# Kernel optimization log

Measured on AMD Instinct MI355X. Metric: run time of the kernel, lower is better.

## Reference

```python
import jax, jax.numpy as jnp
import numpy as np

STEP = 0.01  # matches init kwarg step=0.01


def _disc(x, step=STEP):
    """Discretize like pd.cut with bins arange(floor(min), ceil(max)+step, step).
    Bin identity is all that matters for entropy, so we return integer bin ids.
    (Boundary convention: half-open floor binning; pd.cut uses right-closed,
    which differs only on exact bin edges - measure-zero for continuous data.)"""
    lower = jnp.floor(jnp.min(x))
    return jnp.floor((x - lower) / step).astype(jnp.int32)


def _row_joint_entropy(labels_list):
    """Per-row empirical (joint) entropy in nats of discrete label tuples.
    H_row = -sum_v p_v log p_v = -(1/n) * sum_i log(count(x_i)/n),
    computed via pairwise-equality counts (vectorized Counter).
    labels_list: list of [B, n] int arrays. Returns [B]."""
    eq = None
    for lab in labels_list:
        e = lab[:, :, None] == lab[:, None, :]  # [B, n, n]
        eq = e if eq is None else (eq & e)
    n = labels_list[0].shape[1]
    counts = eq.sum(-1).astype(jnp.float32)  # [B, n]
    return -jnp.mean(jnp.log(counts / n), axis=-1)  # [B]


def _h_soft(o, d):
    """F.cross_entropy(o, softmax(d), 'mean') - F.kl_div(log_softmax(o), softmax(d), 'mean').
    Note torch kl_div 'mean' averages over ALL elements (B*C)."""
    p = jax.nn.softmax(d, axis=-1)
    logq = jax.nn.log_softmax(o, axis=-1)
    ce = -jnp.mean(jnp.sum(p * logq, axis=-1))          # mean over batch
    kl = jnp.mean(p * (jnp.log(p) - logq))               # mean over B*C
    return ce - kl


def reference(data, data1, data2, data3, output1, output2, output3, output):
    # --- reconstruction term ---
    mse_loss = 0.5 * jnp.mean((data - output) ** 2)

    # --- discrete entropies on detached inputs (torch: .detach().numpy()) ---
    d1 = _disc(jax.lax.stop_gradient(data1))
    d2 = _disc(jax.lax.stop_gradient(data2))
    d3 = _disc(jax.lax.stop_gradient(data3))

    H_data_1 = jnp.mean(_row_joint_entropy([d1]))
    H_data_2 = jnp.mean(_row_joint_entropy([d2]))
    H_data_3 = jnp.mean(_row_joint_entropy([d3]))

    H_output_1 = _h_soft(output1, data1)
    H_output_2 = _h_soft(output2, data2)
    H_output_3 = _h_soft(output3, data3)

    H_1 = H_data_1 - H_output_1
    H_2 = H_data_2 - H_output_2
    H_3 = H_data_3 - H_output_3

    # equal widths -> pad_matrices is a no-op
    H_in_1_3 = jnp.mean(_row_joint_entropy([d1, d3]))
    H_in_2_3 = jnp.mean(_row_joint_entropy([d2, d3]))
    H_in_1_2 = jnp.mean(_row_joint_entropy([d1, d2]))

    in1_3 = jnp.concatenate((data1, data3), axis=1)
    in2_3 = jnp.concatenate((data2, data3), axis=1)
    in1_2 = jnp.concatenate((data1, data2), axis=1)
    out1_3 = jnp.concatenate((output1, output3), axis=1)
    out2_3 = jnp.concatenate((output2, output3), axis=1)
    out1_2 = jnp.concatenate((output1, output2), axis=1)

    H_out_1_3 = _h_soft(out1_3, in1_3)
    H_out_2_3 = _h_soft(out2_3, in2_3)
    H_out_1_2 = _h_soft(out1_2, in1_2)

    data1_3 = H_data_1 + H_data_3 - H_in_1_3
    data2_3 = H_data_2 + H_data_3 - H_in_2_3
    data1_2 = H_data_1 + H_data_2 - H_in_1_2
    label1_3 = H_output_1 + H_output_3 - H_out_1_3
    label2_3 = H_output_2 + H_output_3 - H_out_2_3
    label1_2 = H_output_1 + H_output_2 - H_out_1_2

    H_MI1_3 = label1_3 - data1_3
    H_MI2_3 = label2_3 - data2_3
    H_MI1_2 = label1_2 - data1_2

    # per-row conditional MI I(X1; X2 | X3) = H(X1,X3)+H(X2,X3)-H(X3)-H(X1,X2,X3),
    # summed over rows (torch loop accumulates cmi per row without averaging)
    cmi_rows = (_row_joint_entropy([d1, d3]) + _row_joint_entropy([d2, d3])
                - _row_joint_entropy([d3]) - _row_joint_entropy([d1, d2, d3]))
    ave_data_ConMI = jnp.sum(cmi_rows)

    in123 = jnp.concatenate((data1, data2, data3), axis=1)
    out123 = jnp.concatenate((output1, output2, output3), axis=1)
    H_output_123 = _h_soft(out123, in123)
    ave_label_ConMI = H_out_2_3 - H_output_3 + H_out_1_3 - H_output_123
    CMI = ave_label_ConMI - ave_data_ConMI

    return (0.5 * mse_loss
            + 0.25 * (jnp.square(H_1) + jnp.square(H_2) + jnp.square(H_3))
            + 0.25 * (jnp.square(H_MI1_3) + jnp.square(H_MI2_3)
                      + jnp.square(H_MI1_2) + jnp.square(CMI)))


def setup_inputs() -> dict:
    key = jax.random.key(0)
    ks = jax.random.split(key, 8)
    B, D, DT = 2048, 256, 768
    return {
        "data": jax.random.normal(ks[0], (B, DT), dtype=jnp.float32),
        "data1": jax.random.normal(ks[1], (B, D), dtype=jnp.float32),
        "data2": jax.random.normal(ks[2], (B, D), dtype=jnp.float32),
        "data3": jax.random.normal(ks[3], (B, D), dtype=jnp.float32),
        "output1": jax.random.normal(ks[4], (B, D), dtype=jnp.float32),
        "output2": jax.random.normal(ks[5], (B, D), dtype=jnp.float32),
        "output3": jax.random.normal(ks[6], (B, D), dtype=jnp.float32),
        "output": jax.random.normal(ks[7], (B, DT), dtype=jnp.float32),
    }
```

## Files before the change

kernel.cpp:

```cpp
#include <hip/hip_runtime.h>
#include <math.h>

#define B_ROWS 2048
#define NCOL   256
#define DTOT   768
#define BANKS  16
#define HSLOTS 512


#define LO (-6.0f)

__global__ __launch_bounds__(256)
void zero_kernel(double* __restrict__ acc) {
    for (int z = threadIdx.x; z < BANKS * 22; z += 256) acc[z] = 0.0;
}

__device__ __forceinline__ int hslot0(unsigned key) {
    return (int)((key * 0x9E3779B1u) >> 23);
}

__device__ __forceinline__ int hfix(unsigned* __restrict__ h, int slot,
                                    unsigned key, unsigned prev) {
    while (true) {
        if (prev == 0u) return slot;
        if ((prev >> 10) == key) { atomicAdd(&h[slot], 1u); return slot; }
        slot = (slot + 1) & (HSLOTS - 1);
        prev = atomicCAS(&h[slot], 0u, (key << 10) + 1u);
    }
}

__global__ __launch_bounds__(64)
void row_kernel(const float* __restrict__ d1, const float* __restrict__ d2,
                const float* __restrict__ d3,
                const float* __restrict__ o1, const float* __restrict__ o2,
                const float* __restrict__ o3,
                const float* __restrict__ data, const float* __restrict__ outp,
                double* __restrict__ acc) {
    __shared__ unsigned ht[7][HSLOTS];

    const int r = blockIdx.x, lane = threadIdx.x;

    {
        uint4* h4 = (uint4*)&ht[0][0];
        #pragma unroll
        for (int z = 0; z < 14; ++z) h4[lane + z * 64] = make_uint4(0u, 0u, 0u, 0u);
    }

    const float4 X1 = ((const float4*)(d1 + r * NCOL))[lane];
    const float4 X2 = ((const float4*)(d2 + r * NCOL))[lane];
    const float4 X3 = ((const float4*)(d3 + r * NCOL))[lane];
    const float4 Y1 = ((const float4*)(o1 + r * NCOL))[lane];
    const float4 Y2 = ((const float4*)(o2 + r * NCOL))[lane];
    const float4 Y3 = ((const float4*)(o3 + r * NCOL))[lane];
    const float x1[4] = {X1.x, X1.y, X1.z, X1.w};
    const float x2[4] = {X2.x, X2.y, X2.z, X2.w};
    const float x3[4] = {X3.x, X3.y, X3.z, X3.w};
    const float y1[4] = {Y1.x, Y1.y, Y1.z, Y1.w};
    const float y2[4] = {Y2.x, Y2.y, Y2.z, Y2.w};
    const float y3[4] = {Y3.x, Y3.y, Y3.z, Y3.w};

    float ms = 0.f;
    #pragma unroll
    for (int t = 0; t < 3; ++t) {
        const float4 a = ((const float4*)(data + r * DTOT))[lane + 64 * t];
        const float4 o = ((const float4*)(outp + r * DTOT))[lane + 64 * t];
        const float dx = a.x - o.x, dy = a.y - o.y, dz = a.z - o.z, dw = a.w - o.w;
        ms += dx * dx + dy * dy + dz * dz + dw * dw;
    }
    __syncthreads();

    unsigned* t0 = ht[0]; unsigned* t1 = ht[1]; unsigned* t2 = ht[2];
    unsigned* t3 = ht[3]; unsigned* t4 = ht[4]; unsigned* t5 = ht[5];
    unsigned* t6 = ht[6];

    int SL[4][7];
    float sv[12] = {0,0,0,0,0,0,0,0,0,0,0,0};
    #pragma unroll
    for (int j = 0; j < 4; ++j) {
        const unsigned k1 = (unsigned)(int)floorf((x1[j] - LO) / 0.01f);
        const unsigned k2 = (unsigned)(int)floorf((x2[j] - LO) / 0.01f);
        const unsigned k3 = (unsigned)(int)floorf((x3[j] - LO) / 0.01f);
        const unsigned k13 = k1 | (k3 << 11), k23 = k2 | (k3 << 11), k12 = k1 | (k2 << 11);
        int s1 = hslot0(k1), s2 = hslot0(k2), s3 = hslot0(k3);
        int s13 = hslot0(k13), s23 = hslot0(k23), s12 = hslot0(k12);
        const unsigned p1  = atomicCAS(&t0[s1],  0u, (k1  << 10) + 1u);
        const unsigned p2  = atomicCAS(&t1[s2],  0u, (k2  << 10) + 1u);
        const unsigned p3  = atomicCAS(&t2[s3],  0u, (k3  << 10) + 1u);
        const unsigned p13 = atomicCAS(&t3[s13], 0u, (k13 << 10) + 1u);
        const unsigned p23 = atomicCAS(&t4[s23], 0u, (k23 << 10) + 1u);
        const unsigned p12 = atomicCAS(&t5[s12], 0u, (k12 << 10) + 1u);
        SL[j][0] = hfix(t0, s1,  k1,  p1);
        SL[j][1] = hfix(t1, s2,  k2,  p2);
        SL[j][2] = hfix(t2, s3,  k3,  p3);
        s13 = hfix(t3, s13, k13, p13);
        SL[j][3] = s13;
        SL[j][4] = hfix(t4, s23, k23, p23);
        SL[j][5] = hfix(t5, s12, k12, p12);
        const unsigned k123 = (unsigned)s13 | (k2 << 9);
        int s123 = hslot0(k123);
        const unsigned p123 = atomicCAS(&t6[s123], 0u, (k123 << 10) + 1u);
        SL[j][6] = hfix(t6, s123, k123, p123);

        const float ed1 = __expf(x1[j]), ed2 = __expf(x2[j]), ed3 = __expf(x3[j]);
        sv[0] += ed1; sv[1] += ed1 * y1[j]; sv[2]  += ed1 * x1[j]; sv[3]  += __expf(y1[j]);
        sv[4] += ed2; sv[5] += ed2 * y2[j]; sv[6]  += ed2 * x2[j]; sv[7]  += __expf(y2[j]);
        sv[8] += ed3; sv[9] += ed3 * y3[j]; sv[10] += ed3 * x3[j]; sv[11] += __expf(y3[j]);
    }

    float logacc[7] = {0,0,0,0,0,0,0};
    #pragma unroll
    for (int j = 0; j < 4; ++j) {
        logacc[0] += __logf((float)(t0[SL[j][0]] & 1023u));
        logacc[1] += __logf((float)(t1[SL[j][1]] & 1023u));
        logacc[2] += __logf((float)(t2[SL[j][2]] & 1023u));
        logacc[3] += __logf((float)(t3[SL[j][3]] & 1023u));
        logacc[4] += __logf((float)(t4[SL[j][4]] & 1023u));
        logacc[5] += __logf((float)(t5[SL[j][5]] & 1023u));
        logacc[6] += __logf((float)(t6[SL[j][6]] & 1023u));
    }

    float svt[12];
    #pragma unroll
    for (int s = 0; s < 12; ++s) {
        float x = sv[s];
        for (int off = 32; off; off >>= 1) x += __shfl_xor(x, off);
        svt[s] = x;
    }
    float lgt[7];
    #pragma unroll
    for (int s = 0; s < 7; ++s) {
        float x = logacc[s];
        for (int off = 32; off; off >>= 1) x += __shfl_xor(x, off);
        lgt[s] = x;
    }
    float mst = ms;
    for (int off = 32; off; off >>= 1) mst += __shfl_xor(mst, off);

    float fin = mst;
    if (lane < 7) {
        #pragma unroll
        for (int s = 0; s < 7; ++s) fin = (lane == s) ? lgt[s] : fin;
    } else if (lane < 21) {
        const int mi = (lane < 14) ? lane - 7 : lane - 14;
        const int M[7] = {1, 2, 4, 5, 6, 3, 7};
        int mk = 0;
        #pragma unroll
        for (int s = 0; s < 7; ++s) mk = (mi == s) ? M[s] : mk;
        float Zd = 0.f, Td = 0.f, Ud = 0.f, Zo = 0.f;
        #pragma unroll
        for (int k = 0; k < 3; ++k) {
            const float c = (float)((mk >> k) & 1);
            Zd += c * svt[4*k]; Td += c * svt[4*k+1];
            Ud += c * svt[4*k+2]; Zo += c * svt[4*k+3];
        }
        const float Ld = __logf(Zd), Lo = __logf(Zo);
        const float Spo = Td / Zd, Spd = Ud / Zd;
        fin = (lane < 14) ? (Lo - Spo) : ((Spd - Ld) - (Spo - Lo));
    }
    if (lane < 22) atomicAdd(&acc[(r & (BANKS - 1)) * 22 + lane], (double)fin);
}

__global__ __launch_bounds__(64)
void fold_kernel(const double* __restrict__ acc, float* __restrict__ out) {
    __shared__ double T[22];
    const int lane = threadIdx.x;
    if (lane < 22) {
        double s = 0.0;
        #pragma unroll
        for (int bk = 0; bk < BANKS; ++bk) s += acc[bk * 22 + lane];
        T[lane] = s;
    }
    __syncthreads();
    if (lane == 0) {
        const double n = 256.0, Bd = 2048.0;
        const double logn = log(n);
        const double S1 = T[0], S2 = T[1], S3 = T[2];
        const double S13 = T[3], S23 = T[4], S12 = T[5], S123 = T[6];
        const double Hd1   = logn - S1  / (Bd * n);
        const double Hd2   = logn - S2  / (Bd * n);
        const double Hd3   = logn - S3  / (Bd * n);
        const double Hin13 = logn - S13 / (Bd * n);
        const double Hin23 = logn - S23 / (Bd * n);
        const double Hin12 = logn - S12 / (Bd * n);
        const double C[7] = {256, 256, 256, 512, 512, 512, 768};
        double Ho[7];
        for (int m = 0; m < 7; ++m) Ho[m] = T[7 + m] / Bd - T[14 + m] / (Bd * C[m]);
        const double H1 = Hd1 - Ho[0], H2 = Hd2 - Ho[1], H3 = Hd3 - Ho[2];
        const double MI13 = (Ho[0] + Ho[2] - Ho[3]) - (Hd1 + Hd3 - Hin13);
        const double MI23 = (Ho[1] + Ho[2] - Ho[4]) - (Hd2 + Hd3 - Hin23);
        const double MI12 = (Ho[0] + Ho[1] - Ho[5]) - (Hd1 + Hd2 - Hin12);
        const double aveD = -(S13 + S23 - S3 - S123) / n;
        const double aveL = Ho[4] - Ho[2] + Ho[3] - Ho[6];
        const double CMI = aveL - aveD;
        const double mse = 0.5 * T[21] / (Bd * 768.0);
        out[0] = (float)(0.5 * mse
                       + 0.25 * (H1 * H1 + H2 * H2 + H3 * H3)
                       + 0.25 * (MI13 * MI13 + MI23 * MI23 + MI12 * MI12
                                 + CMI * CMI));
    }
}

extern "C" void kernel_launch(void* const* d_in, const int* in_sizes, int n_in,
                              void* d_out, int out_size, void* d_ws, size_t ws_size,
                              hipStream_t stream) {
    const float* data = (const float*)d_in[0];
    const float* d1   = (const float*)d_in[1];
    const float* d2   = (const float*)d_in[2];
    const float* d3   = (const float*)d_in[3];
    const float* o1   = (const float*)d_in[4];
    const float* o2   = (const float*)d_in[5];
    const float* o3   = (const float*)d_in[6];
    const float* outp = (const float*)d_in[7];

    double* acc = (double*)d_ws;

    zero_kernel<<<1, 256, 0, stream>>>(acc);
    row_kernel<<<B_ROWS, 64, 0, stream>>>(d1, d2, d3, o1, o2, o3, data, outp, acc);
    fold_kernel<<<1, 64, 0, stream>>>(acc, (float*)d_out);
}
```

Measured before the change: 102.9 us.

## Use 256-thread blocks per row and write per-row partials instead of atomics

Each row is now processed by 256 threads, one element per thread, instead of 64 threads handling four elements each. The per-row results are reduced through shared memory and written to a per-row workspace slot rather than atomically added into banked double accumulators. This removes the zero kernel and the global double atomics, and the fold kernel now reduces 2048 values per statistic with a 512-thread block. In exchange it adds extra block-wide syncs, uses scalar rather than vector loads, and puts more hash-table contention on each row's 256 threads.

```diff
diff --git a/kernel.cpp b/kernel.cpp
--- a/kernel.cpp
+++ b/kernel.cpp
@@ -4,16 +4,10 @@
 #define B_ROWS 2048
 #define NCOL   256
 #define DTOT   768
-#define BANKS  16
 #define HSLOTS 512
 
-
 #define LO (-6.0f)
 
-__global__ __launch_bounds__(256)
-void zero_kernel(double* __restrict__ acc) {
-    for (int z = threadIdx.x; z < BANKS * 22; z += 256) acc[z] = 0.0;
-}
 
 __device__ __forceinline__ int hslot0(unsigned key) {
     return (int)((key * 0x9E3779B1u) >> 23);
@@ -29,43 +23,39 @@
     }
 }
 
-__global__ __launch_bounds__(64)
+__global__ __launch_bounds__(256)
 void row_kernel(const float* __restrict__ d1, const float* __restrict__ d2,
                 const float* __restrict__ d3,
                 const float* __restrict__ o1, const float* __restrict__ o2,
                 const float* __restrict__ o3,
                 const float* __restrict__ data, const float* __restrict__ outp,
-                double* __restrict__ acc) {
+                double* __restrict__ ws) {
     __shared__ unsigned ht[7][HSLOTS];
-
-    const int r = blockIdx.x, lane = threadIdx.x;
-
-    {
-        uint4* h4 = (uint4*)&ht[0][0];
-        #pragma unroll
-        for (int z = 0; z < 14; ++z) h4[lane + z * 64] = make_uint4(0u, 0u, 0u, 0u);
-    }
-
-    const float4 X1 = ((const float4*)(d1 + r * NCOL))[lane];
-    const float4 X2 = ((const float4*)(d2 + r * NCOL))[lane];
-    const float4 X3 = ((const float4*)(d3 + r * NCOL))[lane];
-    const float4 Y1 = ((const float4*)(o1 + r * NCOL))[lane];
-    const float4 Y2 = ((const float4*)(o2 + r * NCOL))[lane];
-    const float4 Y3 = ((const float4*)(o3 + r * NCOL))[lane];
-    const float x1[4] = {X1.x, X1.y, X1.z, X1.w};
-    const float x2[4] = {X2.x, X2.y, X2.z, X2.w};
-    const float x3[4] = {X3.x, X3.y, X3.z, X3.w};
-    const float y1[4] = {Y1.x, Y1.y, Y1.z, Y1.w};
-    const float y2[4] = {Y2.x, Y2.y, Y2.z, Y2.w};
-    const float y3[4] = {Y3.x, Y3.y, Y3.z, Y3.w};
+    __shared__ float tot[20];
+
+    const int r = blockIdx.x, tid = threadIdx.x;
+    const int lane = tid & 63;
+
+    const float x1 = d1[r * NCOL + tid];
+    const float x2 = d2[r * NCOL + tid];
+    const float x3 = d3[r * NCOL + tid];
+    const float y1 = o1[r * NCOL + tid];
+    const float y2 = o2[r * NCOL + tid];
+    const float y3 = o3[r * NCOL + tid];
 
     float ms = 0.f;
     #pragma unroll
     for (int t = 0; t < 3; ++t) {
-        const float4 a = ((const float4*)(data + r * DTOT))[lane + 64 * t];
-        const float4 o = ((const float4*)(outp + r * DTOT))[lane + 64 * t];
-        const float dx = a.x - o.x, dy = a.y - o.y, dz = a.z - o.z, dw = a.w - o.w;
-        ms += dx * dx + dy * dy + dz * dz + dw * dw;
+        const float a = data[r * DTOT + tid + 256 * t];
+        const float o = outp[r * DTOT + tid + 256 * t];
+        const float dd = a - o;
+        ms += dd * dd;
+    }
+
+    {
+        uint4* h4 = (uint4*)&ht[0][0];
+        for (int z = tid; z < 7 * HSLOTS / 4; z += 256)
+            h4[z] = make_uint4(0u, 0u, 0u, 0u);
     }
     __syncthreads();
 
@@ -73,105 +63,110 @@
     unsigned* t3 = ht[3]; unsigned* t4 = ht[4]; unsigned* t5 = ht[5];
     unsigned* t6 = ht[6];
 
-    int SL[4][7];
-    float sv[12] = {0,0,0,0,0,0,0,0,0,0,0,0};
+    const unsigned k1 = (unsigned)(int)floorf((x1 - LO) / 0.01f);
+    const unsigned k2 = (unsigned)(int)floorf((x2 - LO) / 0.01f);
+    const unsigned k3 = (unsigned)(int)floorf((x3 - LO) / 0.01f);
+    const unsigned k13 = k1 | (k3 << 11), k23 = k2 | (k3 << 11), k12 = k1 | (k2 << 11);
+    int s1 = hslot0(k1), s2 = hslot0(k2), s3 = hslot0(k3);
+    int s13 = hslot0(k13), s23 = hslot0(k23), s12 = hslot0(k12);
+    const unsigned p1  = atomicCAS(&t0[s1],  0u, (k1  << 10) + 1u);
+    const unsigned p2  = atomicCAS(&t1[s2],  0u, (k2  << 10) + 1u);
+    const unsigned p3  = atomicCAS(&t2[s3],  0u, (k3  << 10) + 1u);
+    const unsigned p13 = atomicCAS(&t3[s13], 0u, (k13 << 10) + 1u);
+    const unsigned p23 = atomicCAS(&t4[s23], 0u, (k23 << 10) + 1u);
+    const unsigned p12 = atomicCAS(&t5[s12], 0u, (k12 << 10) + 1u);
+    const int SL0 = hfix(t0, s1,  k1,  p1);
+    const int SL1 = hfix(t1, s2,  k2,  p2);
+    const int SL2 = hfix(t2, s3,  k3,  p3);
+    const int SL3 = hfix(t3, s13, k13, p13);
+    const int SL4 = hfix(t4, s23, k23, p23);
+    const int SL5 = hfix(t5, s12, k12, p12);
+    const unsigned k123 = (unsigned)SL3 | (k2 << 9);
+    int s123 = hslot0(k123);
+    const unsigned p123 = atomicCAS(&t6[s123], 0u, (k123 << 10) + 1u);
+    const int SL6 = hfix(t6, s123, k123, p123);
+
+    float vals[20];
+    const float e1 = __expf(x1), e2 = __expf(x2), e3 = __expf(x3);
+    vals[7]  = e1; vals[8]  = e1 * y1; vals[9]  = e1 * x1; vals[10] = __expf(y1);
+    vals[11] = e2; vals[12] = e2 * y2; vals[13] = e2 * x2; vals[14] = __expf(y2);
+    vals[15] = e3; vals[16] = e3 * y3; vals[17] = e3 * x3; vals[18] = __expf(y3);
+    vals[19] = ms;
+
+    __syncthreads();
+
+    vals[0] = __logf((float)(t0[SL0] & 1023u));
+    vals[1] = __logf((float)(t1[SL1] & 1023u));
+    vals[2] = __logf((float)(t2[SL2] & 1023u));
+    vals[3] = __logf((float)(t3[SL3] & 1023u));
+    vals[4] = __logf((float)(t4[SL4] & 1023u));
+    vals[5] = __logf((float)(t5[SL5] & 1023u));
+    vals[6] = __logf((float)(t6[SL6] & 1023u));
+
     #pragma unroll
-    for (int j = 0; j < 4; ++j) {
-        const unsigned k1 = (unsigned)(int)floorf((x1[j] - LO) / 0.01f);
-        const unsigned k2 = (unsigned)(int)floorf((x2[j] - LO) / 0.01f);
-        const unsigned k3 = (unsigned)(int)floorf((x3[j] - LO) / 0.01f);
-        const unsigned k13 = k1 | (k3 << 11), k23 = k2 | (k3 << 11), k12 = k1 | (k2 << 11);
-        int s1 = hslot0(k1), s2 = hslot0(k2), s3 = hslot0(k3);
-        int s13 = hslot0(k13), s23 = hslot0(k23), s12 = hslot0(k12);
-        const unsigned p1  = atomicCAS(&t0[s1],  0u, (k1  << 10) + 1u);
-        const unsigned p2  = atomicCAS(&t1[s2],  0u, (k2  << 10) + 1u);
-        const unsigned p3  = atomicCAS(&t2[s3],  0u, (k3  << 10) + 1u);
-        const unsigned p13 = atomicCAS(&t3[s13], 0u, (k13 << 10) + 1u);
-        const unsigned p23 = atomicCAS(&t4[s23], 0u, (k23 << 10) + 1u);
-        const unsigned p12 = atomicCAS(&t5[s12], 0u, (k12 << 10) + 1u);
-        SL[j][0] = hfix(t0, s1,  k1,  p1);
-        SL[j][1] = hfix(t1, s2,  k2,  p2);
-        SL[j][2] = hfix(t2, s3,  k3,  p3);
-        s13 = hfix(t3, s13, k13, p13);
-        SL[j][3] = s13;
-        SL[j][4] = hfix(t4, s23, k23, p23);
-        SL[j][5] = hfix(t5, s12, k12, p12);
-        const unsigned k123 = (unsigned)s13 | (k2 << 9);
-        int s123 = hslot0(k123);
-        const unsigned p123 = atomicCAS(&t6[s123], 0u, (k123 << 10) + 1u);
-        SL[j][6] = hfix(t6, s123, k123, p123);
-
-        const float ed1 = __expf(x1[j]), ed2 = __expf(x2[j]), ed3 = __expf(x3[j]);
-        sv[0] += ed1; sv[1] += ed1 * y1[j]; sv[2]  += ed1 * x1[j]; sv[3]  += __expf(y1[j]);
-        sv[4] += ed2; sv[5] += ed2 * y2[j]; sv[6]  += ed2 * x2[j]; sv[7]  += __expf(y2[j]);
-        sv[8] += ed3; sv[9] += ed3 * y3[j]; sv[10] += ed3 * x3[j]; sv[11] += __expf(y3[j]);
-    }
-
-    float logacc[7] = {0,0,0,0,0,0,0};
-    #pragma unroll
-    for (int j = 0; j < 4; ++j) {
-        logacc[0] += __logf((float)(t0[SL[j][0]] & 1023u));
-        logacc[1] += __logf((float)(t1[SL[j][1]] & 1023u));
-        logacc[2] += __logf((float)(t2[SL[j][2]] & 1023u));
-        logacc[3] += __logf((float)(t3[SL[j][3]] & 1023u));
-        logacc[4] += __logf((float)(t4[SL[j][4]] & 1023u));
-        logacc[5] += __logf((float)(t5[SL[j][5]] & 1023u));
-        logacc[6] += __logf((float)(t6[SL[j][6]] & 1023u));
-    }
-
-    float svt[12];
-    #pragma unroll
-    for (int s = 0; s < 12; ++s) {
-        float x = sv[s];
-        for (int off = 32; off; off >>= 1) x += __shfl_xor(x, off);
-        svt[s] = x;
-    }
-    float lgt[7];
-    #pragma unroll
-    for (int s = 0; s < 7; ++s) {
-        float x = logacc[s];
-        for (int off = 32; off; off >>= 1) x += __shfl_xor(x, off);
-        lgt[s] = x;
-    }
-    float mst = ms;
-    for (int off = 32; off; off >>= 1) mst += __shfl_xor(mst, off);
-
-    float fin = mst;
-    if (lane < 7) {
+    for (int v = 0; v < 20; ++v) {
+        float x = vals[v];
+        x += __shfl_xor(x, 1);
+        x += __shfl_xor(x, 2);
+        vals[v] = x;
+    }
+
+    __syncthreads();
+    float* sc = (float*)&ht[0][0];
+    if ((lane & 3) == 0) {
+        const int g = tid >> 2;
         #pragma unroll
-        for (int s = 0; s < 7; ++s) fin = (lane == s) ? lgt[s] : fin;
-    } else if (lane < 21) {
-        const int mi = (lane < 14) ? lane - 7 : lane - 14;
-        const int M[7] = {1, 2, 4, 5, 6, 3, 7};
-        int mk = 0;
+        for (int v = 0; v < 20; ++v) sc[v * 65 + g] = vals[v];
+    }
+    __syncthreads();
+
+    if (tid < 20) {
+        float s = 0.f;
+        for (int g = 0; g < 64; ++g) s += sc[tid * 65 + g];
+        tot[tid] = s;
+    }
+    __syncthreads();
+
+    if (tid < 22) {
+        float fin;
+        if (tid < 7) {
+            fin = tot[tid];
+        } else if (tid == 21) {
+            fin = tot[19];
+        } else {
+            const int mi = (tid < 14) ? tid - 7 : tid - 14;
+            const int M[7] = {1, 2, 4, 5, 6, 3, 7};
+            int mk = 0;
+            #pragma unroll
+            for (int s_ = 0; s_ < 7; ++s_) mk = (mi == s_) ? M[s_] : mk;
+            float Zd = 0.f, Td = 0.f, Ud = 0.f, Zo = 0.f;
+            #pragma unroll
+            for (int k = 0; k < 3; ++k) {
+                const float c = (float)((mk >> k) & 1);
+                Zd += c * tot[7 + 4 * k]; Td += c * tot[8 + 4 * k];
+                Ud += c * tot[9 + 4 * k]; Zo += c * tot[10 + 4 * k];
+            }
+            const float Ld = __logf(Zd), Lo = __logf(Zo);
+            const float Spo = Td / Zd, Spd = Ud / Zd;
+            fin = (tid < 14) ? (Lo - Spo) : ((Spd - Ld) - (Spo - Lo));
+        }
+        ws[tid * B_ROWS + r] = (double)fin;
+    }
+}
+
+__global__ __launch_bounds__(512)
+void fold_kernel(const double* __restrict__ ws, float* __restrict__ out) {
+    __shared__ double T[22];
+    const int tid = threadIdx.x, w = tid >> 6, lane = tid & 63;
+    for (int s = w; s < 22; s += 8) {
+        double acc = 0.0;
         #pragma unroll
-        for (int s = 0; s < 7; ++s) mk = (mi == s) ? M[s] : mk;
-        float Zd = 0.f, Td = 0.f, Ud = 0.f, Zo = 0.f;
-        #pragma unroll
-        for (int k = 0; k < 3; ++k) {
-            const float c = (float)((mk >> k) & 1);
-            Zd += c * svt[4*k]; Td += c * svt[4*k+1];
-            Ud += c * svt[4*k+2]; Zo += c * svt[4*k+3];
-        }
-        const float Ld = __logf(Zd), Lo = __logf(Zo);
-        const float Spo = Td / Zd, Spd = Ud / Zd;
-        fin = (lane < 14) ? (Lo - Spo) : ((Spd - Ld) - (Spo - Lo));
-    }
-    if (lane < 22) atomicAdd(&acc[(r & (BANKS - 1)) * 22 + lane], (double)fin);
-}
-
-__global__ __launch_bounds__(64)
-void fold_kernel(const double* __restrict__ acc, float* __restrict__ out) {
-    __shared__ double T[22];
-    const int lane = threadIdx.x;
-    if (lane < 22) {
-        double s = 0.0;
-        #pragma unroll
-        for (int bk = 0; bk < BANKS; ++bk) s += acc[bk * 22 + lane];
-        T[lane] = s;
-    }
-    __syncthreads();
-    if (lane == 0) {
+        for (int i = 0; i < 32; ++i) acc += ws[s * B_ROWS + lane + 64 * i];
+        for (int off = 32; off; off >>= 1) acc += __shfl_xor(acc, off);
+        if (lane == 0) T[s] = acc;
+    }
+    __syncthreads();
+    if (tid == 0) {
         const double n = 256.0, Bd = 2048.0;
         const double logn = log(n);
         const double S1 = T[0], S2 = T[1], S3 = T[2];
@@ -212,9 +207,8 @@
     const float* o3   = (const float*)d_in[6];
     const float* outp = (const float*)d_in[7];
 
-    double* acc = (double*)d_ws;
-
-    zero_kernel<<<1, 256, 0, stream>>>(acc);
-    row_kernel<<<B_ROWS, 64, 0, stream>>>(d1, d2, d3, o1, o2, o3, data, outp, acc);
-    fold_kernel<<<1, 64, 0, stream>>>(acc, (float*)d_out);
-}
+    double* ws = (double*)d_ws;
+
+    row_kernel<<<B_ROWS, 256, 0, stream>>>(d1, d2, d3, o1, o2, o3, data, outp, ws);
+    fold_kernel<<<1, 512, 0, stream>>>(ws, (float*)d_out);
+}
```

Result: slower. 107.4 us (+4.4%).
